# Kernel tuning notes

Hardware: AMD Instinct MI355X
Metric: run time of the kernel (lower is better)

The kernel has to match this reference:

```python
import jax, jax.numpy as jnp
import numpy as np

C = 1.0          # ball curvature c (manifold k = -c)
RC = 1.0         # sqrt(c)
PROJ_EPS = 4e-3  # geoopt float32 projection eps
NUM_HEADS = 16
B, S, D = 2, 1024, 1024


def _project(x):
    # clip points back inside the Poincare ball
    maxnorm = (1.0 - PROJ_EPS) / RC
    norm = jnp.maximum(jnp.linalg.norm(x, axis=-1, keepdims=True), 1e-15)
    return jnp.where(norm > maxnorm, x / norm * maxnorm, x)


def _poincare_linear(x, z, r, out_split):
    # Unidirectional Poincare MLR (Shimizu et al., HNN++) followed by exp-map back to the ball.
    # x: [..., din]; z: [din, dout]; r: [dout]
    z_norm = jnp.maximum(jnp.linalg.norm(z, axis=0, keepdims=True), 1e-15)  # [1, dout]
    z_unit = z / z_norm
    drcr = 2.0 * RC * r                                    # [dout]
    rcx = RC * x
    cx2 = jnp.sum(rcx * rcx, axis=-1, keepdims=True)       # [..., 1]
    w = 2.0 * (z_norm / RC) * jnp.arcsinh(
        (2.0 * (rcx @ z_unit) * jnp.cosh(drcr) - (1.0 + cx2) * jnp.sinh(drcr))
        / jnp.maximum(1.0 - cx2, 1e-15))
    y = jnp.sinh(RC * w) / RC
    y = y.reshape(y.shape[:-1] + (out_split, y.shape[-1] // out_split))  # [..., H, dh]
    y = _project(y)
    y = y / (1.0 + jnp.sqrt(1.0 + C * jnp.sum(y * y, axis=-1, keepdims=True)))
    return _project(y)


def _dist_matmul(x, y):
    # Pairwise Poincare distance via matmul. x: [..., n, d], y: [..., d, m].
    # dist = (1/sqrt(c)) * arccosh(1 + 2c||x-y||^2 / ((1-c||x||^2)(1-c||y||^2)))
    xy = jnp.matmul(x, y)
    x2 = jnp.sum(x * x, axis=-1, keepdims=True)           # [..., n, 1]
    y2 = jnp.sum(y * y, axis=-2, keepdims=True)           # [..., 1, m]
    num = jnp.maximum(x2 - 2.0 * xy + y2, 1e-15)          # ||x - y||^2
    den = jnp.maximum((1.0 - C * x2) * (1.0 - C * y2), 1e-15)
    return (1.0 / RC) * jnp.arccosh(1.0 + 2.0 * C * num / den)


def _weighted_midpoint_bmm(xs, weights):
    # Weighted Mobius gyromidpoint. xs: [..., n, d], weights: [..., m, n] -> [..., m, d]
    x2 = jnp.sum(xs * xs, axis=-1, keepdims=True)
    gamma = 2.0 / jnp.maximum(1.0 - C * x2, 1e-15)        # conformal factor lambda_x
    denom = jnp.matmul(jnp.abs(weights), gamma - 1.0)     # [..., m, 1]
    nomin = jnp.matmul(weights, gamma * xs)               # [..., m, d]
    two_mean = nomin / jnp.maximum(denom, 1e-10)
    sq = jnp.sum(two_mean * two_mean, axis=-1, keepdims=True)
    a_mean = two_mean / (1.0 + jnp.sqrt(jnp.maximum(1.0 - C * sq, 1e-15)))
    return _project(a_mean)


def setup_inputs() -> dict:
    key = jax.random.key(0)
    ks = jax.random.split(key, 4)
    # points must lie inside the unit ball: ||x|| ~ 0.02*sqrt(D) ~ 0.64
    hidden_states = 0.02 * jax.random.normal(ks[0], (B, S, D), dtype=jnp.float32)
    attention_mask = jnp.zeros((B, 1, 1, S), dtype=jnp.float32)
    scale = 1.0 / np.sqrt(D).astype(np.float32)
    qz = scale * jax.random.normal(ks[1], (D, D), dtype=jnp.float32)
    kz = scale * jax.random.normal(ks[2], (D, D), dtype=jnp.float32)
    vz = scale * jax.random.normal(ks[3], (D, D), dtype=jnp.float32)
    qr = jnp.zeros((D,), jnp.float32)
    kr = jnp.zeros((D,), jnp.float32)
    vr = jnp.zeros((D,), jnp.float32)
    return {"hidden_states": hidden_states, "attention_mask": attention_mask,
            "qz": qz, "qr": qr, "kz": kz, "kr": kr, "vz": vz, "vr": vr}


def reference(hidden_states, attention_mask, qz, qr, kz, kr, vz, vr):
    # self-attention path (encoder_hidden_states is None), eval mode (dropout p=0)
    q = _poincare_linear(hidden_states, qz, qr, NUM_HEADS).transpose(0, 2, 1, 3)  # [B,H,S,dh]
    k = _poincare_linear(hidden_states, kz, kr, NUM_HEADS).transpose(0, 2, 1, 3)
    v = _poincare_linear(hidden_states, vz, vr, NUM_HEADS).transpose(0, 2, 1, 3)
    scores = -_dist_matmul(q, jnp.swapaxes(k, -1, -2)) + attention_mask          # [B,H,S,S]
    probs = jax.nn.softmax(scores, axis=-1)
    ctx = _weighted_midpoint_bmm(v, probs)                                       # [B,H,S,dh]
    b, h, s, dh = ctx.shape
    return ctx.transpose(0, 2, 1, 3).reshape(b, s, h * dh)
```

## Files before the change

kernel.cpp:

```cpp
#include <hip/hip_runtime.h>
#include <math.h>

#define BB 2
#define SS 1024
#define DD 1024
#define NH 16
#define DH 64
#define MAXN 0.996f

typedef __attribute__((ext_vector_type(8))) short bf16x8;
typedef __attribute__((ext_vector_type(4))) float f32x4;

__device__ __forceinline__ float xor_sum16(float v){
  v += __shfl_xor(v, 1, 64);
  v += __shfl_xor(v, 2, 64);
  v += __shfl_xor(v, 4, 64);
  v += __shfl_xor(v, 8, 64);
  return v;
}

__device__ __forceinline__ unsigned short f2bf(float x){
  unsigned u = __builtin_bit_cast(unsigned, x);
  unsigned r = u + 0x7FFFu + ((u >> 16) & 1u);
  return (unsigned short)(r >> 16);
}
__device__ __forceinline__ float bf2f(unsigned short b){
  unsigned u = ((unsigned)b) << 16;
  return __builtin_bit_cast(float, u);
}

__device__ __forceinline__ void async_copy16(const unsigned short* g, unsigned short* s){
  __builtin_amdgcn_global_load_lds(
      (const __attribute__((address_space(1))) unsigned int*)g,
      (__attribute__((address_space(3))) unsigned int*)s,
      16, 0, 0);
}

__global__ __launch_bounds__(256) void col_stats_kernel(
    const float* __restrict__ zq, const float* __restrict__ zk, const float* __restrict__ zv,
    const float* __restrict__ rq, const float* __restrict__ rk, const float* __restrict__ rv,
    float* __restrict__ acol, float* __restrict__ bcol, float* __restrict__ scol)
{
  const int m = blockIdx.y;
  const float* z = (m == 0) ? zq : ((m == 1) ? zk : zv);
  const float* r = (m == 0) ? rq : ((m == 1) ? rk : rv);
  const int col = blockIdx.x * 64 + (threadIdx.x & 63);
  const int slice = threadIdx.x >> 6;
  float acc = 0.0f;
  for (int i = slice * 256; i < slice * 256 + 256; ++i) {
    float t = z[(size_t)i * DD + col]; acc = fmaf(t, t, acc);
  }
  __shared__ float red[4][64];
  red[slice][threadIdx.x & 63] = acc;
  __syncthreads();
  if (slice == 0) {
    const int c = threadIdx.x & 63;
    float a = red[0][c] + red[1][c] + red[2][c] + red[3][c];
    float n = fmaxf(sqrtf(a), 1e-15f);
    float rr = 2.0f * r[col];
    acol[m * DD + col] = 2.0f * coshf(rr) / n;
    bcol[m * DD + col] = sinhf(rr);
    scol[m * DD + col] = 2.0f * n;
  }
}

__global__ __launch_bounds__(256) void row_cx2_kernel(const float* __restrict__ x,
                                                      float* __restrict__ cx2)
{
  const int wave = threadIdx.x >> 6;
  const int lane = threadIdx.x & 63;
  const int row = blockIdx.x * 4 + wave;
  const float* xr = x + (size_t)row * DD;
  float acc = 0.0f;
  for (int i = lane; i < DD; i += 64) { float t = xr[i]; acc = fmaf(t, t, acc); }
  #pragma unroll
  for (int m = 1; m < 64; m <<= 1) acc += __shfl_xor(acc, m, 64);
  if (lane == 0) cx2[row] = acc;
}

__global__ __launch_bounds__(256) void convert_x_kernel(
    const float* __restrict__ x,
    unsigned short* __restrict__ Xhi, unsigned short* __restrict__ Xlo)
{
  const size_t g0 = ((size_t)blockIdx.x * 256 + threadIdx.x) * 8;
  #pragma unroll
  for (int h = 0; h < 2; ++h) {
    float4 v = *(const float4*)(x + g0 + 4 * h);
    float a[4] = {v.x, v.y, v.z, v.w};
    ushort4 hv, lv;
    unsigned short* hp = (unsigned short*)&hv;
    unsigned short* lp = (unsigned short*)&lv;
    #pragma unroll
    for (int j = 0; j < 4; ++j) {
      unsigned short hi = f2bf(a[j]);
      hp[j] = hi;
      lp[j] = f2bf(a[j] - bf2f(hi));
    }
    *(ushort4*)(Xhi + g0 + 4 * h) = hv;
    *(ushort4*)(Xlo + g0 + 4 * h) = lv;
  }
}

__global__ __launch_bounds__(256) void convert_zt_kernel(
    const float* __restrict__ zq, const float* __restrict__ zk, const float* __restrict__ zv,
    unsigned short* __restrict__ ZThi, unsigned short* __restrict__ ZTlo)
{
  const int kt = blockIdx.x, nt = blockIdx.y, mat = blockIdx.z;
  const float* z = (mat == 0) ? zq : ((mat == 1) ? zk : zv);
  const int tid = threadIdx.x;
  __shared__ unsigned T[64][69];

  #pragma unroll
  for (int i = 0; i < 4; ++i) {
    const int g = tid + 256 * i;
    const int kr = g >> 4, nc = (g & 15) * 4;
    float4 v = *(const float4*)(z + (size_t)(kt * 64 + kr) * DD + nt * 64 + nc);
    float a[4] = {v.x, v.y, v.z, v.w};
    #pragma unroll
    for (int j = 0; j < 4; ++j) {
      unsigned short hi = f2bf(a[j]);
      unsigned short lo = f2bf(a[j] - bf2f(hi));
      T[kr][nc + j] = ((unsigned)lo << 16) | (unsigned)hi;
    }
  }
  __syncthreads();
  #pragma unroll
  for (int i = 0; i < 4; ++i) {
    const int g = tid + 256 * i;
    const int nr = g >> 4, kc = (g & 15) * 4;
    ushort4 hv, lv;
    unsigned short* hp = (unsigned short*)&hv;
    unsigned short* lp = (unsigned short*)&lv;
    #pragma unroll
    for (int j = 0; j < 4; ++j) {
      unsigned u = T[kc + j][nr];
      hp[j] = (unsigned short)(u & 0xFFFFu);
      lp[j] = (unsigned short)(u >> 16);
    }
    const size_t ob = ((size_t)mat * DD + nt * 64 + nr) * DD + kt * 64 + kc;
    *(ushort4*)(ZThi + ob) = hv;
    *(ushort4*)(ZTlo + ob) = lv;
  }
}

__global__ __launch_bounds__(256, 3) void gemm_mfma_kernel(
    const unsigned short* __restrict__ Xhi, const unsigned short* __restrict__ Xlo,
    const unsigned short* __restrict__ ZThi, const unsigned short* __restrict__ ZTlo,
    const float* __restrict__ acol, const float* __restrict__ bcol, const float* __restrict__ scol,
    const float* __restrict__ cx2,
    unsigned short* __restrict__ Qhi, unsigned short* __restrict__ Qlo,
    unsigned short* __restrict__ Khi, unsigned short* __restrict__ Klo,
    float* __restrict__ GV,
    float* __restrict__ q2, float* __restrict__ k2, float* __restrict__ gm1)
{
  __shared__ unsigned short S[2][12288];

  const int mat = blockIdx.z;
  float* Stat = (mat == 0) ? q2 : ((mat == 1) ? k2 : gm1);
  unsigned short* Bh = (mat == 0) ? Qhi : Khi;
  unsigned short* Bl = (mat == 0) ? Qlo : Klo;

  const int n0 = blockIdx.x * 128;
  const int m0 = blockIdx.y * 64;
  const int tid = threadIdx.x;
  const int wave = tid >> 6, lane = tid & 63;
  const int tx = lane & 15, quad = lane >> 4;
  const int wrow = wave & 1;
  const int wcol = wave >> 1;

  const int l4r = lane >> 2, l4c = (lane & 3) * 8;
  auto slice_ptr = [&](int si) -> const unsigned short* {
    if (si < 8) {
      const unsigned short* base = (si < 4) ? Xhi : Xlo;
      const int r16 = (si & 3) * 16;
      return base + (size_t)(m0 + r16 + l4r) * DD + l4c;
    } else {
      const unsigned short* base = (si < 16) ? ZThi : ZTlo;
      const int r16 = ((si - 8) & 7) * 16;
      return base + ((size_t)mat * DD + n0 + r16 + l4r) * DD + l4c;
    }
  };
  const int s0 = 6 * wave;
  const unsigned short* p0 = slice_ptr(s0 + 0);
  const unsigned short* p1 = slice_ptr(s0 + 1);
  const unsigned short* p2 = slice_ptr(s0 + 2);
  const unsigned short* p3 = slice_ptr(s0 + 3);
  const unsigned short* p4 = slice_ptr(s0 + 4);
  const unsigned short* p5 = slice_ptr(s0 + 5);
  const int o0 = 512 * (s0 + 0), o1 = 512 * (s0 + 1), o2 = 512 * (s0 + 2);
  const int o3 = 512 * (s0 + 3), o4 = 512 * (s0 + 4), o5 = 512 * (s0 + 5);

  const f32x4 z4 = {0.f, 0.f, 0.f, 0.f};
  f32x4 d00 = z4, d01 = z4, d02 = z4, d03 = z4;
  f32x4 d10 = z4, d11 = z4, d12 = z4, d13 = z4;

  async_copy16(p0, &S[0][o0]); async_copy16(p1, &S[0][o1]); async_copy16(p2, &S[0][o2]);
  async_copy16(p3, &S[0][o3]); async_copy16(p4, &S[0][o4]); async_copy16(p5, &S[0][o5]);
  p0 += 32; p1 += 32; p2 += 32; p3 += 32; p4 += 32; p5 += 32;

  for (int kt = 0; kt < 32; ++kt) {
    __syncthreads();
    if (kt < 31) {
      unsigned short* Bn = S[(kt + 1) & 1];
      async_copy16(p0, Bn + o0); async_copy16(p1, Bn + o1); async_copy16(p2, Bn + o2);
      async_copy16(p3, Bn + o3); async_copy16(p4, Bn + o4); async_copy16(p5, Bn + o5);
      p0 += 32; p1 += 32; p2 += 32; p3 += 32; p4 += 32; p5 += 32;
    }
    const unsigned short* Bc = S[kt & 1];
    const int ar = 32 * wrow + tx;
    bf16x8 a_h0 = *(const bf16x8*)&Bc[ar * 32 + 8 * quad];
    bf16x8 a_l0 = *(const bf16x8*)&Bc[2048 + ar * 32 + 8 * quad];
    bf16x8 a_h1 = *(const bf16x8*)&Bc[(ar + 16) * 32 + 8 * quad];
    bf16x8 a_l1 = *(const bf16x8*)&Bc[2048 + (ar + 16) * 32 + 8 * quad];

#define DO_NB(NB, C0, C1) { \
      const int brow = 16 * (4 * wcol + NB) + tx; \
      bf16x8 b_h = *(const bf16x8*)&Bc[4096 + brow * 32 + 8 * quad]; \
      bf16x8 b_l = *(const bf16x8*)&Bc[8192 + brow * 32 + 8 * quad]; \
      C0 = __builtin_amdgcn_mfma_f32_16x16x32_bf16(a_h0, b_h, C0, 0, 0, 0); \
      C0 = __builtin_amdgcn_mfma_f32_16x16x32_bf16(a_h0, b_l, C0, 0, 0, 0); \
      C0 = __builtin_amdgcn_mfma_f32_16x16x32_bf16(a_l0, b_h, C0, 0, 0, 0); \
      C1 = __builtin_amdgcn_mfma_f32_16x16x32_bf16(a_h1, b_h, C1, 0, 0, 0); \
      C1 = __builtin_amdgcn_mfma_f32_16x16x32_bf16(a_h1, b_l, C1, 0, 0, 0); \
      C1 = __builtin_amdgcn_mfma_f32_16x16x32_bf16(a_l1, b_h, C1, 0, 0, 0); }
    DO_NB(0, d00, d10)
    DO_NB(1, d01, d11)
    DO_NB(2, d02, d12)
    DO_NB(3, d03, d13)
#undef DO_NB
  }

  const int head = blockIdx.x * 2 + wcol;
  #pragma unroll
  for (int mb = 0; mb < 2; ++mb) {
    const f32x4 e0 = mb ? d10 : d00;
    const f32x4 e1 = mb ? d11 : d01;
    const f32x4 e2 = mb ? d12 : d02;
    const f32x4 e3 = mb ? d13 : d03;
    #pragma unroll
    for (int r = 0; r < 4; ++r) {
      const int row = m0 + 32 * wrow + 16 * mb + 4 * quad + r;
      const float c2 = cx2[row];
      const float inv = 1.0f / fmaxf(1.0f - c2, 1e-15f);
      const float onec = 1.0f + c2;
      float yv[4];
      #pragma unroll
      for (int nb = 0; nb < 4; ++nb) {
        const float accv = (nb == 0) ? e0[r] : (nb == 1) ? e1[r] : (nb == 2) ? e2[r] : e3[r];
        const int col = mat * DD + n0 + 64 * wcol + 16 * nb + tx;
        const float u = fmaf(accv, acol[col], -(onec * bcol[col])) * inv;
        const float a = fabsf(u);
        const float t = a + sqrtf(fmaf(a, a, 1.0f));
        const float p = __builtin_amdgcn_exp2f(scol[col] * __builtin_amdgcn_logf(t));
        float y = 0.5f * (p - __builtin_amdgcn_rcpf(p));
        yv[nb] = copysignf(y, u);
      }
      const int b = row >> 10, s = row & 1023;
      float n2 = 0.f;
      #pragma unroll
      for (int j = 0; j < 4; ++j) n2 = fmaf(yv[j], yv[j], n2);
      n2 = xor_sum16(n2);
      float n = fmaxf(sqrtf(n2), 1e-15f);
      float s1 = (n > MAXN) ? (MAXN / n) : 1.0f;
      n2 = n2 * s1 * s1;
      float f = 1.0f / (1.0f + sqrtf(1.0f + n2));
      float fs = s1 * f;
      n2 = n2 * f * f;
      float nb2 = fmaxf(sqrtf(n2), 1e-15f);
      float s2f = (nb2 > MAXN) ? (MAXN / nb2) : 1.0f;
      fs *= s2f;
      n2 = n2 * s2f * s2f;

      const size_t bh = (size_t)(b * NH + head);
      const size_t outbase = (bh * SS + s) * DH;
      if (mat == 2) {
        const float gamma = 2.0f / fmaxf(1.0f - n2, 1e-15f);
        #pragma unroll
        for (int j = 0; j < 4; ++j)
          GV[outbase + 16 * j + tx] = yv[j] * fs * gamma;
        if (tx == 0) Stat[bh * SS + s] = gamma - 1.0f;
      } else {
        #pragma unroll
        for (int j = 0; j < 4; ++j) {
          const float v = yv[j] * fs;
          const unsigned short hi = f2bf(v);
          const unsigned short lo = f2bf(v - bf2f(hi));
          Bh[outbase + 16 * j + tx] = hi;
          Bl[outbase + 16 * j + tx] = lo;
        }
        if (tx == 0) Stat[bh * SS + s] = n2;
      }
    }
  }
}

__global__ __launch_bounds__(256) void convert_gt_kernel(
    const float* __restrict__ GV,
    unsigned short* __restrict__ GThi, unsigned short* __restrict__ GTlo)
{
  const int st = blockIdx.x, bh = blockIdx.y;
  const int tid = threadIdx.x;
  const float* src = GV + ((size_t)bh * SS + st * 64) * DH;
  __shared__ unsigned T[64][69];

  #pragma unroll
  for (int i = 0; i < 4; ++i) {
    const int g = tid + 256 * i;
    const int row = g >> 4, c4 = (g & 15) * 4;
    float4 v = *(const float4*)(src + row * DH + c4);
    float a[4] = {v.x, v.y, v.z, v.w};
    #pragma unroll
    for (int j = 0; j < 4; ++j) {
      unsigned short hi = f2bf(a[j]);
      unsigned short lo = f2bf(a[j] - bf2f(hi));
      T[row][c4 + j] = ((unsigned)lo << 16) | (unsigned)hi;
    }
  }
  __syncthreads();
  #pragma unroll
  for (int i = 0; i < 4; ++i) {
    const int g = tid + 256 * i;
    const int kb = g & 15, dhr = g >> 4;
    ushort4 hv, lv;
    unsigned short* hp = (unsigned short*)&hv;
    unsigned short* lp = (unsigned short*)&lv;
    #pragma unroll
    for (int j = 0; j < 4; ++j) {
      unsigned u = T[4 * kb + j][dhr];
      hp[j] = (unsigned short)(u & 0xFFFFu);
      lp[j] = (unsigned short)(u >> 16);
    }
    const size_t ob = ((size_t)bh * DH + dhr) * SS + st * 64 + 4 * kb;
    *(ushort4*)(GThi + ob) = hv;
    *(ushort4*)(GTlo + ob) = lv;
  }
}

__global__ __launch_bounds__(256) void flash_attn_kernel(
    const unsigned short* __restrict__ Qhi, const unsigned short* __restrict__ Qlo,
    const unsigned short* __restrict__ Khi, const unsigned short* __restrict__ Klo,
    const unsigned short* __restrict__ GThi, const unsigned short* __restrict__ GTlo,
    const float* __restrict__ q2a, const float* __restrict__ k2a, const float* __restrict__ gm1a,
    const float* __restrict__ mask, float* __restrict__ out)
{
  constexpr int LDK = 72;
  __shared__ unsigned short Ks_hi[64 * LDK];
  __shared__ unsigned short Ks_lo[64 * LDK];
  __shared__ unsigned short Gs_hi[64 * LDK];
  __shared__ unsigned short Gs_lo[64 * LDK];
  __shared__ unsigned short Ps_hi[64 * LDK];
  __shared__ unsigned short Ps_lo[64 * LDK];
  __shared__ float k2s[64], ik2s[64], gm1s[64], ems[64];

  const int qt = blockIdx.x, h = blockIdx.y, b = blockIdx.z;
  const int bh = b * NH + h;
  const int tid = threadIdx.x;
  const int wave = tid >> 6, lane = tid & 63;
  const int tx = lane & 15, quad = lane >> 4;
  const int r0 = qt * 64;

  bf16x8 qa_h[2], qa_l[2];
  {
    const size_t qoff = ((size_t)bh * SS + r0 + 16 * wave + tx) * DH;
    #pragma unroll
    for (int kc = 0; kc < 2; ++kc) {
      qa_h[kc] = *(const bf16x8*)(Qhi + qoff + 32 * kc + 8 * quad);
      qa_l[kc] = *(const bf16x8*)(Qlo + qoff + 32 * kc + 8 * quad);
    }
  }
  float q2r[4], iq2[4];
  #pragma unroll
  for (int r = 0; r < 4; ++r) {
    q2r[r] = q2a[(size_t)bh * SS + r0 + 16 * wave + 4 * quad + r];
    iq2[r] = 2.0f / fmaxf(1.0f - q2r[r], 1e-15f);
  }

  const f32x4 zero4 = {0.f, 0.f, 0.f, 0.f};
  f32x4 oacc[4] = {zero4, zero4, zero4, zero4};
  float dden[4] = {0.f, 0.f, 0.f, 0.f};

  const int c0 = tid, c1 = tid + 256;
  const int sr0 = c0 >> 3, sc0 = (c0 & 7) * 8;
  const int sr1 = c1 >> 3, sc1 = (c1 & 7) * 8;

  const size_t kbase = (size_t)bh * SS * DH;
  const size_t gbase = (size_t)bh * DH * SS;

  uint4 pk_h0 = *(const uint4*)(Khi + kbase + (size_t)sr0 * DH + sc0);
  uint4 pk_h1 = *(const uint4*)(Khi + kbase + (size_t)sr1 * DH + sc1);
  uint4 pk_l0 = *(const uint4*)(Klo + kbase + (size_t)sr0 * DH + sc0);
  uint4 pk_l1 = *(const uint4*)(Klo + kbase + (size_t)sr1 * DH + sc1);
  uint4 pg_h0 = *(const uint4*)(GThi + gbase + (size_t)sr0 * SS + sc0);
  uint4 pg_h1 = *(const uint4*)(GThi + gbase + (size_t)sr1 * SS + sc1);
  uint4 pg_l0 = *(const uint4*)(GTlo + gbase + (size_t)sr0 * SS + sc0);
  uint4 pg_l1 = *(const uint4*)(GTlo + gbase + (size_t)sr1 * SS + sc1);
  float p_k2 = 0.f, p_gm1 = 0.f, p_ms = 0.f;
  if (tid < 64) {
    p_k2  = k2a[(size_t)bh * SS + tid];
    p_gm1 = gm1a[(size_t)bh * SS + tid];
    p_ms  = mask[(size_t)b * SS + tid];
  }

  for (int kt = 0; kt < 16; ++kt) {
    __syncthreads();
    *(uint4*)&Ks_hi[sr0 * LDK + sc0] = pk_h0;
    *(uint4*)&Ks_hi[sr1 * LDK + sc1] = pk_h1;
    *(uint4*)&Ks_lo[sr0 * LDK + sc0] = pk_l0;
    *(uint4*)&Ks_lo[sr1 * LDK + sc1] = pk_l1;
    *(uint4*)&Gs_hi[sr0 * LDK + sc0] = pg_h0;
    *(uint4*)&Gs_hi[sr1 * LDK + sc1] = pg_h1;
    *(uint4*)&Gs_lo[sr0 * LDK + sc0] = pg_l0;
    *(uint4*)&Gs_lo[sr1 * LDK + sc1] = pg_l1;
    if (tid < 64) {
      k2s[tid]  = p_k2;
      ik2s[tid] = 1.0f / fmaxf(1.0f - p_k2, 1e-15f);
      gm1s[tid] = p_gm1;
      ems[tid]  = __expf(p_ms);
    }
    __syncthreads();
    if (kt < 15) {
      const int t1 = (kt + 1) * 64;
      const size_t kb_ = kbase + (size_t)t1 * DH;
      const size_t gb_ = gbase + t1;
      pk_h0 = *(const uint4*)(Khi + kb_ + (size_t)sr0 * DH + sc0);
      pk_h1 = *(const uint4*)(Khi + kb_ + (size_t)sr1 * DH + sc1);
      pk_l0 = *(const uint4*)(Klo + kb_ + (size_t)sr0 * DH + sc0);
      pk_l1 = *(const uint4*)(Klo + kb_ + (size_t)sr1 * DH + sc1);
      pg_h0 = *(const uint4*)(GThi + gb_ + (size_t)sr0 * SS + sc0);
      pg_h1 = *(const uint4*)(GThi + gb_ + (size_t)sr1 * SS + sc1);
      pg_l0 = *(const uint4*)(GTlo + gb_ + (size_t)sr0 * SS + sc0);
      pg_l1 = *(const uint4*)(GTlo + gb_ + (size_t)sr1 * SS + sc1);
      if (tid < 64) {
        p_k2  = k2a[(size_t)bh * SS + t1 + tid];
        p_gm1 = gm1a[(size_t)bh * SS + t1 + tid];
        p_ms  = mask[(size_t)b * SS + t1 + tid];
      }
    }

    f32x4 sacc[4] = {zero4, zero4, zero4, zero4};
    #pragma unroll
    for (int kc = 0; kc < 2; ++kc) {
      const int ko = 32 * kc + 8 * quad;
      #pragma unroll
      for (int nb = 0; nb < 4; ++nb) {
        bf16x8 kh = *(const bf16x8*)&Ks_hi[(16 * nb + tx) * LDK + ko];
        bf16x8 kl = *(const bf16x8*)&Ks_lo[(16 * nb + tx) * LDK + ko];
        sacc[nb] = __builtin_amdgcn_mfma_f32_16x16x32_bf16(qa_h[kc], kh, sacc[nb], 0, 0, 0);
        sacc[nb] = __builtin_amdgcn_mfma_f32_16x16x32_bf16(qa_h[kc], kl, sacc[nb], 0, 0, 0);
        sacc[nb] = __builtin_amdgcn_mfma_f32_16x16x32_bf16(qa_l[kc], kh, sacc[nb], 0, 0, 0);
      }
    }

    float pb[4][4];
    #pragma unroll
    for (int nb = 0; nb < 4; ++nb) {
      const int key = 16 * nb + tx;
      const float k2v = k2s[key], ikv = ik2s[key], emv = ems[key], gmv = gm1s[key];
      #pragma unroll
      for (int r = 0; r < 4; ++r) {
        float sv = sacc[nb][r];
        float num = fmaxf(fmaf(-2.0f, sv, q2r[r] + k2v), 1e-15f);
        float e = num * iq2[r] * ikv;
        float g = fmaf(e, e, e + e);
        float z = 1.0f + e + __builtin_amdgcn_sqrtf(g);
        float w = emv * __builtin_amdgcn_rcpf(z);
        pb[r][nb] = w;
        dden[r] = fmaf(w, gmv, dden[r]);
      }
    }

    #pragma unroll
    for (int r = 0; r < 4; ++r) {
      const int prow = 16 * wave + 4 * quad + r;
      #pragma unroll
      for (int nb = 0; nb < 4; ++nb) {
        float w = pb[r][nb];
        unsigned short hi = f2bf(w);
        unsigned short lo = f2bf(w - bf2f(hi));
        Ps_hi[prow * LDK + 16 * nb + tx] = hi;
        Ps_lo[prow * LDK + 16 * nb + tx] = lo;
      }
    }
    #pragma unroll
    for (int kc = 0; kc < 2; ++kc) {
      const int ko = 32 * kc + 8 * quad;
      bf16x8 ph = *(const bf16x8*)&Ps_hi[(16 * wave + tx) * LDK + ko];
      bf16x8 pl = *(const bf16x8*)&Ps_lo[(16 * wave + tx) * LDK + ko];
      #pragma unroll
      for (int nb = 0; nb < 4; ++nb) {
        bf16x8 gh = *(const bf16x8*)&Gs_hi[(16 * nb + tx) * LDK + ko];
        bf16x8 gl = *(const bf16x8*)&Gs_lo[(16 * nb + tx) * LDK + ko];
        oacc[nb] = __builtin_amdgcn_mfma_f32_16x16x32_bf16(ph, gh, oacc[nb], 0, 0, 0);
        oacc[nb] = __builtin_amdgcn_mfma_f32_16x16x32_bf16(ph, gl, oacc[nb], 0, 0, 0);
        oacc[nb] = __builtin_amdgcn_mfma_f32_16x16x32_bf16(pl, gh, oacc[nb], 0, 0, 0);
      }
    }
  }

  #pragma unroll
  for (int r = 0; r < 4; ++r) {
    float d = fmaxf(xor_sum16(dden[r]), 1e-10f);
    float invd = 1.0f / d;
    float tm[4]; float sq = 0.f;
    #pragma unroll
    for (int nb = 0; nb < 4; ++nb) { tm[nb] = oacc[nb][r] * invd; sq = fmaf(tm[nb], tm[nb], sq); }
    sq = xor_sum16(sq);
    const float f = 1.0f / (1.0f + sqrtf(fmaxf(1.0f - sq, 1e-15f)));
    const float n2 = sq * f * f;
    const float n = fmaxf(sqrtf(n2), 1e-15f);
    const float s2 = (n > MAXN) ? (MAXN / n) : 1.0f;
    const float fs = f * s2;
    const int qrow = r0 + 16 * wave + 4 * quad + r;
    #pragma unroll
    for (int nb = 0; nb < 4; ++nb)
      out[((size_t)(b * SS + qrow)) * DD + h * DH + 16 * nb + tx] = tm[nb] * fs;
  }
}

extern "C" void kernel_launch(void* const* d_in, const int* in_sizes, int n_in,
                              void* d_out, int out_size, void* d_ws, size_t ws_size,
                              hipStream_t stream) {
  const float* hs   = (const float*)d_in[0];
  const float* mask = (const float*)d_in[1];
  const float* qz   = (const float*)d_in[2];
  const float* qr   = (const float*)d_in[3];
  const float* kz   = (const float*)d_in[4];
  const float* kr   = (const float*)d_in[5];
  const float* vz   = (const float*)d_in[6];
  const float* vr   = (const float*)d_in[7];
  float* out = (float*)d_out;

  float* ws = (float*)d_ws;
  const size_t nQKV = (size_t)BB * NH * SS * DH;
  const size_t nStat = (size_t)BB * NH * SS;

  float* GV  = ws;
  float* q2  = GV + nQKV;
  float* k2  = q2 + nStat;
  float* gm1 = k2 + nStat;
  float* acol = gm1 + nStat;
  float* bcol = acol + 3 * DD;
  float* scol = bcol + 3 * DD;
  float* cx2 = scol + 3 * DD;

  unsigned short* sb  = (unsigned short*)(cx2 + 2048);
  unsigned short* Qhi  = sb;
  unsigned short* Qlo  = Qhi + nQKV;
  unsigned short* Khi  = Qlo + nQKV;
  unsigned short* Klo  = Khi + nQKV;
  unsigned short* GThi = Klo + nQKV;
  unsigned short* GTlo = GThi + nQKV;
  unsigned short* Xhi  = GThi;
  unsigned short* Xlo  = GTlo;
  unsigned short* ZThi = GTlo + nQKV;
  unsigned short* ZTlo = ZThi + 3 * (size_t)DD * DD;

  col_stats_kernel<<<dim3(16, 3), 256, 0, stream>>>(qz, kz, vz, qr, kr, vr, acol, bcol, scol);
  row_cx2_kernel<<<dim3(512), 256, 0, stream>>>(hs, cx2);
  convert_x_kernel<<<dim3(1024), 256, 0, stream>>>(hs, Xhi, Xlo);
  convert_zt_kernel<<<dim3(16, 16, 3), 256, 0, stream>>>(qz, kz, vz, ZThi, ZTlo);
  gemm_mfma_kernel<<<dim3(8, 32, 3), 256, 0, stream>>>(
      Xhi, Xlo, ZThi, ZTlo, acol, bcol, scol, cx2,
      Qhi, Qlo, Khi, Klo, GV, q2, k2, gm1);
  convert_gt_kernel<<<dim3(16, BB * NH), 256, 0, stream>>>(GV, GThi, GTlo);
  flash_attn_kernel<<<dim3(16, NH, BB), 256, 0, stream>>>(
      Qhi, Qlo, Khi, Klo, GThi, GTlo, q2, k2, gm1, mask, out);
}
```

Before: 229.7 us.

## Fuse prep kernels into one launch and fold V transpose into GEMM epilogue

Merges col_stats, row_cx2, convert_x and convert_zt into a single prep kernel that dispatches on block index, and computes the row norm of x while converting it. The GEMM epilogue for the V matrix now splits values into bf16 hi/lo and transposes them through shared memory, writing GThi/GTlo directly, which removes the fp32 GV buffer and the separate convert_gt kernel. The aim is to cut launch count and a full fp32 round trip through global memory. The cost is extra shared-memory traffic and barriers in the GEMM epilogue for the V blocks, and new workspace regions for X because it no longer aliases GT.

```diff
diff --git a/kernel.cpp b/kernel.cpp
--- a/kernel.cpp
+++ b/kernel.cpp
@@ -36,110 +36,106 @@
       16, 0, 0);
 }
 
-__global__ __launch_bounds__(256) void col_stats_kernel(
+__global__ __launch_bounds__(256) void prep_kernel(
+    const float* __restrict__ hs,
     const float* __restrict__ zq, const float* __restrict__ zk, const float* __restrict__ zv,
     const float* __restrict__ rq, const float* __restrict__ rk, const float* __restrict__ rv,
-    float* __restrict__ acol, float* __restrict__ bcol, float* __restrict__ scol)
-{
-  const int m = blockIdx.y;
-  const float* z = (m == 0) ? zq : ((m == 1) ? zk : zv);
-  const float* r = (m == 0) ? rq : ((m == 1) ? rk : rv);
-  const int col = blockIdx.x * 64 + (threadIdx.x & 63);
-  const int slice = threadIdx.x >> 6;
-  float acc = 0.0f;
-  for (int i = slice * 256; i < slice * 256 + 256; ++i) {
-    float t = z[(size_t)i * DD + col]; acc = fmaf(t, t, acc);
-  }
-  __shared__ float red[4][64];
-  red[slice][threadIdx.x & 63] = acc;
-  __syncthreads();
-  if (slice == 0) {
-    const int c = threadIdx.x & 63;
-    float a = red[0][c] + red[1][c] + red[2][c] + red[3][c];
-    float n = fmaxf(sqrtf(a), 1e-15f);
-    float rr = 2.0f * r[col];
-    acol[m * DD + col] = 2.0f * coshf(rr) / n;
-    bcol[m * DD + col] = sinhf(rr);
-    scol[m * DD + col] = 2.0f * n;
-  }
-}
-
-__global__ __launch_bounds__(256) void row_cx2_kernel(const float* __restrict__ x,
-                                                      float* __restrict__ cx2)
-{
-  const int wave = threadIdx.x >> 6;
-  const int lane = threadIdx.x & 63;
-  const int row = blockIdx.x * 4 + wave;
-  const float* xr = x + (size_t)row * DD;
-  float acc = 0.0f;
-  for (int i = lane; i < DD; i += 64) { float t = xr[i]; acc = fmaf(t, t, acc); }
-  #pragma unroll
-  for (int m = 1; m < 64; m <<= 1) acc += __shfl_xor(acc, m, 64);
-  if (lane == 0) cx2[row] = acc;
-}
-
-__global__ __launch_bounds__(256) void convert_x_kernel(
-    const float* __restrict__ x,
-    unsigned short* __restrict__ Xhi, unsigned short* __restrict__ Xlo)
-{
-  const size_t g0 = ((size_t)blockIdx.x * 256 + threadIdx.x) * 8;
-  #pragma unroll
-  for (int h = 0; h < 2; ++h) {
-    float4 v = *(const float4*)(x + g0 + 4 * h);
-    float a[4] = {v.x, v.y, v.z, v.w};
-    ushort4 hv, lv;
-    unsigned short* hp = (unsigned short*)&hv;
-    unsigned short* lp = (unsigned short*)&lv;
-    #pragma unroll
-    for (int j = 0; j < 4; ++j) {
-      unsigned short hi = f2bf(a[j]);
-      hp[j] = hi;
-      lp[j] = f2bf(a[j] - bf2f(hi));
-    }
-    *(ushort4*)(Xhi + g0 + 4 * h) = hv;
-    *(ushort4*)(Xlo + g0 + 4 * h) = lv;
-  }
-}
-
-__global__ __launch_bounds__(256) void convert_zt_kernel(
-    const float* __restrict__ zq, const float* __restrict__ zk, const float* __restrict__ zv,
+    float* __restrict__ acol, float* __restrict__ bcol, float* __restrict__ scol,
+    float* __restrict__ cx2,
+    unsigned short* __restrict__ Xhi, unsigned short* __restrict__ Xlo,
     unsigned short* __restrict__ ZThi, unsigned short* __restrict__ ZTlo)
 {
-  const int kt = blockIdx.x, nt = blockIdx.y, mat = blockIdx.z;
-  const float* z = (mat == 0) ? zq : ((mat == 1) ? zk : zv);
+  __shared__ unsigned shbuf[64 * 69];
+  const int bid = blockIdx.x;
   const int tid = threadIdx.x;
-  __shared__ unsigned T[64][69];
-
-  #pragma unroll
-  for (int i = 0; i < 4; ++i) {
-    const int g = tid + 256 * i;
-    const int kr = g >> 4, nc = (g & 15) * 4;
-    float4 v = *(const float4*)(z + (size_t)(kt * 64 + kr) * DD + nt * 64 + nc);
-    float a[4] = {v.x, v.y, v.z, v.w};
-    #pragma unroll
-    for (int j = 0; j < 4; ++j) {
-      unsigned short hi = f2bf(a[j]);
-      unsigned short lo = f2bf(a[j] - bf2f(hi));
-      T[kr][nc + j] = ((unsigned)lo << 16) | (unsigned)hi;
-    }
-  }
-  __syncthreads();
-  #pragma unroll
-  for (int i = 0; i < 4; ++i) {
-    const int g = tid + 256 * i;
-    const int nr = g >> 4, kc = (g & 15) * 4;
-    ushort4 hv, lv;
-    unsigned short* hp = (unsigned short*)&hv;
-    unsigned short* lp = (unsigned short*)&lv;
-    #pragma unroll
-    for (int j = 0; j < 4; ++j) {
-      unsigned u = T[kc + j][nr];
-      hp[j] = (unsigned short)(u & 0xFFFFu);
-      lp[j] = (unsigned short)(u >> 16);
-    }
-    const size_t ob = ((size_t)mat * DD + nt * 64 + nr) * DD + kt * 64 + kc;
-    *(ushort4*)(ZThi + ob) = hv;
-    *(ushort4*)(ZTlo + ob) = lv;
+
+  if (bid < 48) {
+    const int m = bid >> 4, xb = bid & 15;
+    const float* z = (m == 0) ? zq : ((m == 1) ? zk : zv);
+    const float* r = (m == 0) ? rq : ((m == 1) ? rk : rv);
+    const int col = xb * 64 + (tid & 63);
+    const int slice = tid >> 6;
+    float acc = 0.0f;
+    for (int i = slice * 256; i < slice * 256 + 256; ++i) {
+      float t = z[(size_t)i * DD + col]; acc = fmaf(t, t, acc);
+    }
+    float (*red)[64] = (float(*)[64])shbuf;
+    red[slice][tid & 63] = acc;
+    __syncthreads();
+    if (slice == 0) {
+      const int c = tid & 63;
+      float a = red[0][c] + red[1][c] + red[2][c] + red[3][c];
+      float n = fmaxf(sqrtf(a), 1e-15f);
+      float rr = 2.0f * r[col];
+      acol[m * DD + col] = 2.0f * coshf(rr) / n;
+      bcol[m * DD + col] = sinhf(rr);
+      scol[m * DD + col] = 2.0f * n;
+    }
+  } else if (bid < 48 + 1024) {
+    const int b = bid - 48;
+    const size_t g0 = (size_t)b * 2048 + (size_t)tid * 8;
+    float acc = 0.0f;
+    #pragma unroll
+    for (int h = 0; h < 2; ++h) {
+      float4 v = *(const float4*)(hs + g0 + 4 * h);
+      float a[4] = {v.x, v.y, v.z, v.w};
+      ushort4 hv, lv;
+      unsigned short* hp = (unsigned short*)&hv;
+      unsigned short* lp = (unsigned short*)&lv;
+      #pragma unroll
+      for (int j = 0; j < 4; ++j) {
+        acc = fmaf(a[j], a[j], acc);
+        unsigned short hi = f2bf(a[j]);
+        hp[j] = hi;
+        lp[j] = f2bf(a[j] - bf2f(hi));
+      }
+      *(ushort4*)(Xhi + g0 + 4 * h) = hv;
+      *(ushort4*)(Xlo + g0 + 4 * h) = lv;
+    }
+    #pragma unroll
+    for (int m = 1; m < 64; m <<= 1) acc += __shfl_xor(acc, m, 64);
+    float* red = (float*)shbuf;
+    const int wave = tid >> 6, lane = tid & 63;
+    if (lane == 0) red[wave] = acc;
+    __syncthreads();
+    if (tid == 0)   cx2[2 * b]     = red[0] + red[1];
+    if (tid == 128) cx2[2 * b + 1] = red[2] + red[3];
+  } else {
+    const int b2 = bid - 1072;
+    const int kt = b2 & 15, nt = (b2 >> 4) & 15, mat = b2 >> 8;
+    const float* z = (mat == 0) ? zq : ((mat == 1) ? zk : zv);
+    unsigned (*T)[69] = (unsigned(*)[69])shbuf;
+    #pragma unroll
+    for (int i = 0; i < 4; ++i) {
+      const int g = tid + 256 * i;
+      const int kr = g >> 4, nc = (g & 15) * 4;
+      float4 v = *(const float4*)(z + (size_t)(kt * 64 + kr) * DD + nt * 64 + nc);
+      float a[4] = {v.x, v.y, v.z, v.w};
+      #pragma unroll
+      for (int j = 0; j < 4; ++j) {
+        unsigned short hi = f2bf(a[j]);
+        unsigned short lo = f2bf(a[j] - bf2f(hi));
+        T[kr][nc + j] = ((unsigned)lo << 16) | (unsigned)hi;
+      }
+    }
+    __syncthreads();
+    #pragma unroll
+    for (int i = 0; i < 4; ++i) {
+      const int g = tid + 256 * i;
+      const int nr = g >> 4, kc = (g & 15) * 4;
+      ushort4 hv, lv;
+      unsigned short* hp = (unsigned short*)&hv;
+      unsigned short* lp = (unsigned short*)&lv;
+      #pragma unroll
+      for (int j = 0; j < 4; ++j) {
+        unsigned u = T[kc + j][nr];
+        hp[j] = (unsigned short)(u & 0xFFFFu);
+        lp[j] = (unsigned short)(u >> 16);
+      }
+      const size_t ob = ((size_t)mat * DD + nt * 64 + nr) * DD + kt * 64 + kc;
+      *(ushort4*)(ZThi + ob) = hv;
+      *(ushort4*)(ZTlo + ob) = lv;
+    }
   }
 }
 
@@ -150,7 +146,7 @@
     const float* __restrict__ cx2,
     unsigned short* __restrict__ Qhi, unsigned short* __restrict__ Qlo,
     unsigned short* __restrict__ Khi, unsigned short* __restrict__ Klo,
-    float* __restrict__ GV,
+    unsigned short* __restrict__ GThi, unsigned short* __restrict__ GTlo,
     float* __restrict__ q2, float* __restrict__ k2, float* __restrict__ gm1)
 {
   __shared__ unsigned short S[2][12288];
@@ -231,6 +227,9 @@
   }
 
   const int head = blockIdx.x * 2 + wcol;
+  unsigned* Tr = (unsigned*)&S[0][0];
+  if (mat == 2) __syncthreads();
+
   #pragma unroll
   for (int mb = 0; mb < 2; ++mb) {
     const f32x4 e0 = mb ? d10 : d00;
@@ -239,7 +238,8 @@
     const f32x4 e3 = mb ? d13 : d03;
     #pragma unroll
     for (int r = 0; r < 4; ++r) {
-      const int row = m0 + 32 * wrow + 16 * mb + 4 * quad + r;
+      const int sl = 32 * wrow + 16 * mb + 4 * quad + r;
+      const int row = m0 + sl;
       const float c2 = cx2[row];
       const float inv = 1.0f / fmaxf(1.0f - c2, 1e-15f);
       const float onec = 1.0f + c2;
@@ -276,8 +276,12 @@
       if (mat == 2) {
         const float gamma = 2.0f / fmaxf(1.0f - n2, 1e-15f);
         #pragma unroll
-        for (int j = 0; j < 4; ++j)
-          GV[outbase + 16 * j + tx] = yv[j] * fs * gamma;
+        for (int j = 0; j < 4; ++j) {
+          const float v = yv[j] * fs * gamma;
+          const unsigned short hi = f2bf(v);
+          const unsigned short lo = f2bf(v - bf2f(hi));
+          Tr[(wcol * 64 + sl) * 65 + 16 * j + tx] = ((unsigned)lo << 16) | (unsigned)hi;
+        }
         if (tx == 0) Stat[bh * SS + s] = gamma - 1.0f;
       } else {
         #pragma unroll
@@ -292,47 +296,31 @@
       }
     }
   }
-}
-
-__global__ __launch_bounds__(256) void convert_gt_kernel(
-    const float* __restrict__ GV,
-    unsigned short* __restrict__ GThi, unsigned short* __restrict__ GTlo)
-{
-  const int st = blockIdx.x, bh = blockIdx.y;
-  const int tid = threadIdx.x;
-  const float* src = GV + ((size_t)bh * SS + st * 64) * DH;
-  __shared__ unsigned T[64][69];
-
-  #pragma unroll
-  for (int i = 0; i < 4; ++i) {
-    const int g = tid + 256 * i;
-    const int row = g >> 4, c4 = (g & 15) * 4;
-    float4 v = *(const float4*)(src + row * DH + c4);
-    float a[4] = {v.x, v.y, v.z, v.w};
-    #pragma unroll
-    for (int j = 0; j < 4; ++j) {
-      unsigned short hi = f2bf(a[j]);
-      unsigned short lo = f2bf(a[j] - bf2f(hi));
-      T[row][c4 + j] = ((unsigned)lo << 16) | (unsigned)hi;
-    }
-  }
-  __syncthreads();
-  #pragma unroll
-  for (int i = 0; i < 4; ++i) {
-    const int g = tid + 256 * i;
-    const int kb = g & 15, dhr = g >> 4;
-    ushort4 hv, lv;
-    unsigned short* hp = (unsigned short*)&hv;
-    unsigned short* lp = (unsigned short*)&lv;
-    #pragma unroll
-    for (int j = 0; j < 4; ++j) {
-      unsigned u = T[4 * kb + j][dhr];
-      hp[j] = (unsigned short)(u & 0xFFFFu);
-      lp[j] = (unsigned short)(u >> 16);
-    }
-    const size_t ob = ((size_t)bh * DH + dhr) * SS + st * 64 + 4 * kb;
-    *(ushort4*)(GThi + ob) = hv;
-    *(ushort4*)(GTlo + ob) = lv;
+
+  if (mat == 2) {
+    __syncthreads();
+    const int bb = m0 >> 10, sbase = m0 & 1023;
+    #pragma unroll
+    for (int i = 0; i < 2; ++i) {
+      const int task = tid + 256 * i;
+      const int rowid = task >> 2;
+      const int hh = rowid >> 6, dh = rowid & 63;
+      const int sc = (task & 3) * 16;
+      unsigned short hbuf[16] __attribute__((aligned(16)));
+      unsigned short lbuf[16] __attribute__((aligned(16)));
+      #pragma unroll
+      for (int s = 0; s < 16; ++s) {
+        unsigned u = Tr[(hh * 64 + sc + s) * 65 + dh];
+        hbuf[s] = (unsigned short)(u & 0xFFFFu);
+        lbuf[s] = (unsigned short)(u >> 16);
+      }
+      const int hg = blockIdx.x * 2 + hh;
+      const size_t ob = (((size_t)(bb * NH + hg)) * DH + dh) * SS + sbase + sc;
+      *(uint4*)(GThi + ob)     = *(uint4*)&hbuf[0];
+      *(uint4*)(GThi + ob + 8) = *(uint4*)&hbuf[8];
+      *(uint4*)(GTlo + ob)     = *(uint4*)&lbuf[0];
+      *(uint4*)(GTlo + ob + 8) = *(uint4*)&lbuf[8];
+    }
   }
 }
 
@@ -534,8 +522,7 @@
   const size_t nQKV = (size_t)BB * NH * SS * DH;
   const size_t nStat = (size_t)BB * NH * SS;
 
-  float* GV  = ws;
-  float* q2  = GV + nQKV;
+  float* q2  = ws;
   float* k2  = q2 + nStat;
   float* gm1 = k2 + nStat;
   float* acol = gm1 + nStat;
@@ -543,26 +530,23 @@
   float* scol = bcol + 3 * DD;
   float* cx2 = scol + 3 * DD;
 
-  unsigned short* sb  = (unsigned short*)(cx2 + 2048);
+  unsigned short* sb   = (unsigned short*)(cx2 + 2048);
   unsigned short* Qhi  = sb;
   unsigned short* Qlo  = Qhi + nQKV;
   unsigned short* Khi  = Qlo + nQKV;
   unsigned short* Klo  = Khi + nQKV;
   unsigned short* GThi = Klo + nQKV;
   unsigned short* GTlo = GThi + nQKV;
-  unsigned short* Xhi  = GThi;
-  unsigned short* Xlo  = GTlo;
-  unsigned short* ZThi = GTlo + nQKV;
+  unsigned short* Xhi  = GTlo + nQKV;
+  unsigned short* Xlo  = Xhi + nQKV;
+  unsigned short* ZThi = Xlo + nQKV;
   unsigned short* ZTlo = ZThi + 3 * (size_t)DD * DD;
 
-  col_stats_kernel<<<dim3(16, 3), 256, 0, stream>>>(qz, kz, vz, qr, kr, vr, acol, bcol, scol);
-  row_cx2_kernel<<<dim3(512), 256, 0, stream>>>(hs, cx2);
-  convert_x_kernel<<<dim3(1024), 256, 0, stream>>>(hs, Xhi, Xlo);
-  convert_zt_kernel<<<dim3(16, 16, 3), 256, 0, stream>>>(qz, kz, vz, ZThi, ZTlo);
+  prep_kernel<<<dim3(1840), 256, 0, stream>>>(
+      hs, qz, kz, vz, qr, kr, vr, acol, bcol, scol, cx2, Xhi, Xlo, ZThi, ZTlo);
   gemm_mfma_kernel<<<dim3(8, 32, 3), 256, 0, stream>>>(
       Xhi, Xlo, ZThi, ZTlo, acol, bcol, scol, cx2,
-      Qhi, Qlo, Khi, Klo, GV, q2, k2, gm1);
-  convert_gt_kernel<<<dim3(16, BB * NH), 256, 0, stream>>>(GV, GThi, GTlo);
+      Qhi, Qlo, Khi, Klo, GThi, GTlo, q2, k2, gm1);
   flash_attn_kernel<<<dim3(16, NH, BB), 256, 0, stream>>>(
       Qhi, Qlo, Khi, Klo, GThi, GTlo, q2, k2, gm1, mask, out);
 }
```

New measurement: 208.3 us. -9.3%, faster.
